# Kernel optimization log

Hardware: AMD Instinct MI355X
Metric: run time of the kernel (lower is better)

## Reference

```python
import jax, jax.numpy as jnp
import numpy as np

N = 100000      # nodes
E = 1600000     # edges (before self loops)
IN_DIM, EMB, HID, OUT, L = 128, 128, 128, 64, 3
LN_EPS = 1e-5


def _lin(k, fi, fo):
    return (jax.random.normal(k, (fi, fo), jnp.float32) / np.sqrt(fi)).astype(jnp.float32)


def setup_inputs() -> dict:
    key = jax.random.key(0)
    ks = jax.random.split(key, 8)
    x = jax.random.normal(ks[0], (N, IN_DIM), jnp.float32)
    edge_index = jax.random.randint(ks[1], (2, E), 0, N, dtype=jnp.int64)
    # in-degree of destination nodes (as data.degree would provide)
    degree = jnp.zeros((N,), jnp.float32).at[edge_index[1]].add(1.0)
    lks = jax.random.split(ks[2], 2 * L)
    W1 = jnp.stack([_lin(lks[2 * i], EMB, HID) for i in range(L)])
    W2 = jnp.stack([_lin(lks[2 * i + 1], HID, EMB) for i in range(L)])
    return dict(
        x=x, edge_index=edge_index, degree=degree,
        Win=_lin(ks[3], IN_DIM, EMB), b_in=jnp.zeros((EMB,), jnp.float32),
        W1=W1, b1=jnp.zeros((L, HID), jnp.float32),
        W2=W2, b2=jnp.zeros((L, EMB), jnp.float32),
        ln_g=jnp.ones((L, EMB), jnp.float32), ln_b=jnp.zeros((L, EMB), jnp.float32),
        out_g=jnp.ones((EMB,), jnp.float32), out_b=jnp.zeros((EMB,), jnp.float32),
        Wout=_lin(ks[4], EMB, OUT), b_out=jnp.zeros((OUT,), jnp.float32),
    )


def _layernorm(h, g, b):
    m = h.mean(-1, keepdims=True)
    v = ((h - m) ** 2).mean(-1, keepdims=True)
    return (h - m) * jax.lax.rsqrt(v + LN_EPS) * g + b


def reference(x, edge_index, degree, Win, b_in, W1, b1, W2, b2,
              ln_g, ln_b, out_g, out_b, Wout, b_out):
    # input_lin: Linear -> Dropout(eval: identity) -> ReLU
    h = jax.nn.relu(x @ Win + b_in)                        # [N, EMB]
    # add self loops, degree + 1
    loop = jnp.arange(N, dtype=edge_index.dtype)
    src = jnp.concatenate([edge_index[0], loop])           # [E+N]
    dst = jnp.concatenate([edge_index[1], loop])
    inv = jax.lax.rsqrt(degree + 1.0)                      # deg^{-1/2}
    coef = (inv[src] * inv[dst])[:, None]                  # symmetric GCN norm
    for i in range(L):
        m = h @ W1[i] + b1[i]                              # [N, HID]
        agg = jax.ops.segment_sum(m[src] * coef, dst, num_segments=N)  # gather-scatter
        out = agg @ W2[i] + b2[i]                          # [N, EMB]
        h = jax.nn.relu(_layernorm(out + h, ln_g[i], ln_b[i]))  # residual + LN + act (dropout=id)
    h = _layernorm(h, out_g, out_b)
    return h @ Wout + b_out
```

## Files before the change

### kernel.cpp

```cpp
#include <hip/hip_runtime.h>
#include <cstdint>
#include <cstddef>

typedef unsigned short u16;
typedef unsigned int u32;
typedef __attribute__((ext_vector_type(2))) unsigned short u16x2;
typedef __attribute__((ext_vector_type(4))) unsigned short u16x4;
typedef __attribute__((ext_vector_type(8))) unsigned short u16x8;
typedef __attribute__((ext_vector_type(8))) __bf16 bf16x8;
typedef __attribute__((ext_vector_type(4))) float f32x4;

#define PREP_F32   0
#define PREP_BF16  1
#define PREP_LN    2
#define EPI_IN    0
#define EPI_SCALE 1
#define EPI_NONE  3

__device__ __forceinline__ float wred(float v) {
#pragma unroll
  for (int m = 32; m >= 1; m >>= 1) v += __shfl_xor(v, m, 64);
  return v;
}
__device__ __forceinline__ u16 f2bf(float f) {
  u32 u = __float_as_uint(f);
  u += 0x7fffu + ((u >> 16) & 1u);
  return (u16)(u >> 16);
}
__device__ __forceinline__ float bflo(u32 u) { return __uint_as_float(u << 16); }
__device__ __forceinline__ float bfhi(u32 u) { return __uint_as_float(u & 0xffff0000u); }
__device__ __forceinline__ u32 pack2(float a, float b) {
  u32 ua = __float_as_uint(a); ua += 0x7fffu + ((ua >> 16) & 1u);
  u32 ub = __float_as_uint(b); ub += 0x7fffu + ((ub >> 16) & 1u);
  return (ua >> 16) | (ub & 0xffff0000u);
}


template <int NOUT, int PREP, int EPI>
__device__ __forceinline__ void gemm_body(
    const void* __restrict__ Xv, const u16* __restrict__ Wp,
    const float* __restrict__ bias, void* __restrict__ Yv,
    const void* __restrict__ resv, const float* __restrict__ g1,
    const float* __restrict__ lb1, int N, int bid) {
  constexpr int NT = NOUT / 16;
  __shared__ union {
    u16  xs[32][136];
    float cs[32][132];
  } sh;
  const int tid = threadIdx.x;
  const int lane = tid & 63, wid = tid >> 6;
  const int row0 = bid * 32;

  if constexpr (PREP == PREP_F32) {
    const float* X = (const float*)Xv;
    for (int i = tid; i < 1024; i += 256) {
      int r = i >> 5, c4 = i & 31;
      float4 v = ((const float4*)(X + (size_t)(row0 + r) * 128))[c4];
      u16x4 o = {f2bf(v.x), f2bf(v.y), f2bf(v.z), f2bf(v.w)};
      *(u16x4*)&sh.xs[r][c4 * 4] = o;
    }
  } else if constexpr (PREP == PREP_BF16) {
    const u16x4* X = (const u16x4*)Xv;
    for (int i = tid; i < 1024; i += 256) {
      int r = i >> 5, c4 = i & 31;
      *(u16x4*)&sh.xs[r][c4 * 4] = X[(size_t)(row0 + r) * 32 + c4];
    }
  } else {
    const u32* X = (const u32*)Xv;
    float2 gg = *(const float2*)&g1[lane * 2];
    float2 bb = *(const float2*)&lb1[lane * 2];
    for (int rr = 0; rr < 8; ++rr) {
      int r = wid * 8 + rr;
      u32 v = X[(size_t)(row0 + r) * 64 + lane];
      float tx = bflo(v), ty = bfhi(v);
      float mean = wred(tx + ty) * (1.f / 128.f);
      float dx = tx - mean, dy = ty - mean;
      float var = wred(dx * dx + dy * dy) * (1.f / 128.f);
      float rstd = rsqrtf(var + 1e-5f);
      u16x2 o = {f2bf(dx * rstd * gg.x + bb.x), f2bf(dy * rstd * gg.y + bb.y)};
      *(u16x2*)&sh.xs[r][lane * 2] = o;
    }
  }
  __syncthreads();

  constexpr int NTW = (NOUT == 128) ? 4 : 2;
  const int m0  = (NOUT == 128) ? ((wid >> 1) << 4) : ((wid & 1) << 4);
  const int ntb = (NOUT == 128) ? ((wid & 1) << 2) : ((wid >> 1) << 1);

  f32x4 acc[NTW];
#pragma unroll
  for (int t = 0; t < NTW; ++t) acc[t] = (f32x4){0.f, 0.f, 0.f, 0.f};

  const int ar  = m0 + (lane & 15);
  const int akb = (lane >> 4) << 2;
  const bf16x8* Bp = (const bf16x8*)Wp;
#pragma unroll
  for (int kc = 0; kc < 4; ++kc) {
    u16x4 lo = *(const u16x4*)&sh.xs[ar][kc * 32 + akb];
    u16x4 hi = *(const u16x4*)&sh.xs[ar][kc * 32 + akb + 16];
    u16x8 av;
#pragma unroll
    for (int j = 0; j < 4; ++j) { av[j] = lo[j]; av[j + 4] = hi[j]; }
    bf16x8 a = __builtin_bit_cast(bf16x8, av);
#pragma unroll
    for (int t = 0; t < NTW; ++t) {
      bf16x8 b = Bp[(kc * NT + ntb + t) * 64 + lane];
      acc[t] = __builtin_amdgcn_mfma_f32_16x16x32_bf16(a, b, acc[t], 0, 0, 0);
    }
  }

  const int cb = lane & 15;
  const int rg = (lane >> 4) << 2;
  if constexpr (EPI == EPI_NONE) {
    float* Y = (float*)Yv;
#pragma unroll
    for (int t = 0; t < NTW; ++t) {
      int col = (ntb + t) * 16 + cb;
      float bv = bias[col];
#pragma unroll
      for (int r = 0; r < 4; ++r) {
        int gr = row0 + m0 + rg + r;
        Y[(size_t)gr * NOUT + col] = acc[t][r] + bv;
      }
    }
  } else if constexpr (EPI == EPI_SCALE) {
    const float* inv = (const float*)resv;
    u16* Y = (u16*)Yv;
#pragma unroll
    for (int t = 0; t < NTW; ++t) {
      int col = (ntb + t) * 16 + cb;
      float bv = bias[col];
#pragma unroll
      for (int r = 0; r < 4; ++r) {
        int gr = row0 + m0 + rg + r;
        Y[(size_t)gr * NOUT + col] = f2bf((acc[t][r] + bv) * inv[gr]);
      }
    }
  } else {
    __syncthreads();
#pragma unroll
    for (int t = 0; t < NTW; ++t) {
      int col = (ntb + t) * 16 + cb;
      float bv = bias[col];
#pragma unroll
      for (int r = 0; r < 4; ++r) sh.cs[m0 + rg + r][col] = acc[t][r] + bv;
    }
    __syncthreads();
    u32* Y = (u32*)Yv;
    for (int rr = 0; rr < 8; ++rr) {
      int r = wid * 8 + rr;
      int gr = row0 + r;
      float2 t2 = *(const float2*)&sh.cs[r][lane * 2];
      Y[(size_t)gr * 64 + lane] = pack2(fmaxf(t2.x, 0.f), fmaxf(t2.y, 0.f));
    }
  }
}


__global__ __launch_bounds__(256) void d1_scan_pack_k(
    const float* __restrict__ deg, int* __restrict__ offs,
    int* __restrict__ bsum, float* __restrict__ inv, int N, int nb,
    const float* __restrict__ Win, const float* __restrict__ W1,
    const float* __restrict__ W2, const float* __restrict__ Wout,
    u16* __restrict__ pWin, u16* __restrict__ pW1,
    u16* __restrict__ pW2, u16* __restrict__ pWout) {
  if ((int)blockIdx.x < nb) {
    __shared__ int sh[256];
    int tid = threadIdx.x;
    int i = blockIdx.x * 256 + tid;
    int c = (i < N) ? (int)(deg[i] + 0.5f) : 0;
    if (i < N) inv[i] = rsqrtf(deg[i] + 1.0f);
    int val = c;
    for (int off = 1; off < 256; off <<= 1) {
      sh[tid] = val; __syncthreads();
      if (tid >= off) val += sh[tid - off];
      __syncthreads();
    }
    if (i < N) offs[i] = val - c;
    if (tid == 255) bsum[blockIdx.x] = val;
    return;
  }
  const int b = blockIdx.x - nb;
  const float* W; u16* P; int ncol; int t;
  if (b < 8)       { W = Win;                        P = pWin;                      ncol = 128; t = b * 256 + threadIdx.x; }
  else if (b < 32) { int l = (b - 8) / 8;  W = W1 + (size_t)l * 16384;  P = pW1 + (size_t)l * 16384; ncol = 128; t = ((b - 8) % 8) * 256 + threadIdx.x; }
  else if (b < 56) { int l = (b - 32) / 8; W = W2 + (size_t)l * 16384;  P = pW2 + (size_t)l * 16384; ncol = 128; t = ((b - 32) % 8) * 256 + threadIdx.x; }
  else             { W = Wout;                       P = pWout;                     ncol = 64;  t = (b - 56) * 256 + threadIdx.x; }
  int NT = ncol >> 4;
  int total = 4 * NT * 64;
  if (t >= total) return;
  int lane = t & 63;
  int tmp = t >> 6;
  int nt = tmp % NT, kc = tmp / NT;
  int n = nt * 16 + (lane & 15);
  int kb = kc * 32 + ((lane >> 4) << 2);
  u16* dst = P + (size_t)t * 8;
#pragma unroll
  for (int j = 0; j < 8; ++j) {
    int k = kb + (j & 3) + ((j >> 2) << 4);
    dst[j] = f2bf(W[(size_t)k * ncol + n]);
  }
}

__global__ __launch_bounds__(256) void d2_gemmin_bsum_k(
    const void* __restrict__ Xv, const u16* __restrict__ Wp,
    const float* __restrict__ bias, void* __restrict__ Yv, int N,
    int* __restrict__ bsum, int nb) {
  if (blockIdx.x == gridDim.x - 1) {
    __shared__ int a[512], b[512];
    int tid = threadIdx.x;
    for (int i = tid; i < 512; i += 256) a[i] = (i < nb) ? bsum[i] : 0;
    __syncthreads();
    int* src = a; int* dst = b;
    for (int off = 1; off < 512; off <<= 1) {
      for (int i = tid; i < 512; i += 256)
        dst[i] = (i >= off) ? src[i] + src[i - off] : src[i];
      __syncthreads();
      int* t = src; src = dst; dst = t;
    }
    for (int i = tid; i < nb; i += 256) bsum[i] = (i > 0) ? src[i - 1] : 0;
    return;
  }
  gemm_body<128, PREP_F32, EPI_IN>(Xv, Wp, bias, Yv, nullptr, nullptr, nullptr,
                                   N, blockIdx.x);
}

__global__ __launch_bounds__(256) void d3_gemmscale_scanadd_k(
    const void* __restrict__ Xv, const u16* __restrict__ Wp,
    const float* __restrict__ bias, void* __restrict__ Yv,
    const float* __restrict__ inv, int N,
    int* __restrict__ offs, const int* __restrict__ bsum,
    int* __restrict__ gcur, int E, int gemmGrid) {
  if ((int)blockIdx.x >= gemmGrid) {
    int i = (blockIdx.x - gemmGrid) * 256 + threadIdx.x;
    if (i < N) {
      int o = offs[i] + bsum[i >> 8];
      offs[i] = o;
      if ((i & 511) == 0) gcur[i >> 9] = o;
    } else if (i == N) {
      offs[N] = E;
    }
    return;
  }
  gemm_body<128, PREP_BF16, EPI_SCALE>(Xv, Wp, bias, Yv, inv, nullptr, nullptr,
                                       N, blockIdx.x);
}

template <int NOUT, int PREP, int EPI>
__global__ __launch_bounds__(256) void gemm_mfma(
    const void* __restrict__ Xv, const u16* __restrict__ Wp,
    const float* __restrict__ bias, void* __restrict__ Yv,
    const void* __restrict__ resv, const float* __restrict__ g1,
    const float* __restrict__ lb1, int N) {
  gemm_body<NOUT, PREP, EPI>(Xv, Wp, bias, Yv, resv, g1, lb1, N, blockIdx.x);
}

__global__ __launch_bounds__(256) void scatter_k(
    const int* __restrict__ src, const int* __restrict__ dst,
    int* __restrict__ gcur, u32* __restrict__ pairs, int E) {
  __shared__ int hist[256];
  __shared__ int base_[256];
  const int tid = threadIdx.x;
  const int e0 = blockIdx.x * 8192;
  const int e1 = min(E, e0 + 8192);
  hist[tid] = 0;
  __syncthreads();
  for (int e = e0 + tid; e < e1; e += 256)
    atomicAdd(&hist[dst[e] >> 9], 1);
  __syncthreads();
  int c = hist[tid];
  if (c > 0) base_[tid] = atomicAdd(&gcur[tid], c);
  hist[tid] = 0;
  __syncthreads();
  for (int e = e0 + tid; e < e1; e += 256) {
    int d = dst[e];
    int b = d >> 9;
    int r = atomicAdd(&hist[b], 1);
    pairs[base_[b] + r] = (u32)src[e] | ((u32)(d & 511) << 17);
  }
}

__global__ __launch_bounds__(256) void fill2_k(
    const u32* __restrict__ pairs, const int* __restrict__ offs,
    int* __restrict__ col, int N) {
  __shared__ int cur[512];
  const int b = blockIdx.x;
  const int n0 = b << 9;
  const int n1 = min(N, n0 + 512);
  const int tid = threadIdx.x;
  for (int i = tid; i < n1 - n0; i += 256) cur[i] = offs[n0 + i];
  __syncthreads();
  const int e0 = offs[n0], e1 = offs[n1];
  for (int e = e0 + tid; e < e1; e += 256) {
    u32 pr = pairs[e];
    int p = atomicAdd(&cur[pr >> 17], 1);
    col[p] = (int)(pr & 0x1FFFFu);
  }
}

__global__ __launch_bounds__(256) void spmm_gemm_k(
    const uint4* __restrict__ msc, const int* __restrict__ offs,
    const int* __restrict__ col, const float* __restrict__ inv,
    const u16* __restrict__ Wp, const float* __restrict__ bias,
    u32* __restrict__ h, const float* __restrict__ g1,
    const float* __restrict__ lb1, int N) {
  __shared__ union {
    u16  xs[32][136];
    float cs[16][132];
  } sh;
  const int tid = threadIdx.x;
  const int lane = tid & 63, wid = tid >> 6;
  const int row0 = blockIdx.x * 32;
  const int rgrp = lane >> 4, c = lane & 15;

#pragma unroll
  for (int p = 0; p < 2; ++p) {
    const int lrow = wid * 8 + p * 4 + rgrp;
    const int d = row0 + lrow;
    const int s0 = offs[d], s1 = offs[d + 1];
    const int last = s1 - 1;
    float2 a0 = {0.f, 0.f}, a1 = {0.f, 0.f}, a2 = {0.f, 0.f}, a3 = {0.f, 0.f};
    for (int k = s0; k < s1; k += 8) {
      int sv[8];
#pragma unroll
      for (int j = 0; j < 8; ++j) sv[j] = col[min(k + j, last)];
      uint4 rv[8];
#pragma unroll
      for (int j = 0; j < 8; ++j) rv[j] = msc[(size_t)sv[j] * 16 + c];
#pragma unroll
      for (int j = 0; j < 8; ++j) {
        float m = (k + j < s1) ? 1.f : 0.f;
        a0.x = fmaf(m, bflo(rv[j].x), a0.x); a0.y = fmaf(m, bfhi(rv[j].x), a0.y);
        a1.x = fmaf(m, bflo(rv[j].y), a1.x); a1.y = fmaf(m, bfhi(rv[j].y), a1.y);
        a2.x = fmaf(m, bflo(rv[j].z), a2.x); a2.y = fmaf(m, bfhi(rv[j].z), a2.y);
        a3.x = fmaf(m, bflo(rv[j].w), a3.x); a3.y = fmaf(m, bfhi(rv[j].w), a3.y);
      }
    }
    uint4 r = msc[(size_t)d * 16 + c];
    float iv = inv[d];
    uint4 o;
    o.x = pack2((a0.x + bflo(r.x)) * iv, (a0.y + bfhi(r.x)) * iv);
    o.y = pack2((a1.x + bflo(r.y)) * iv, (a1.y + bfhi(r.y)) * iv);
    o.z = pack2((a2.x + bflo(r.z)) * iv, (a2.y + bfhi(r.z)) * iv);
    o.w = pack2((a3.x + bflo(r.w)) * iv, (a3.y + bfhi(r.w)) * iv);
    *(uint4*)&sh.xs[lrow][c * 8] = o;
  }
  __syncthreads();

  const int m0  = (wid >> 1) << 4;
  const int ntb = (wid & 1) << 2;
  f32x4 acc[4];
#pragma unroll
  for (int t = 0; t < 4; ++t) acc[t] = (f32x4){0.f, 0.f, 0.f, 0.f};
  const int ar  = m0 + (lane & 15);
  const int akb = (lane >> 4) << 2;
  const bf16x8* Bp = (const bf16x8*)Wp;
#pragma unroll
  for (int kc = 0; kc < 4; ++kc) {
    u16x4 lo = *(const u16x4*)&sh.xs[ar][kc * 32 + akb];
    u16x4 hi = *(const u16x4*)&sh.xs[ar][kc * 32 + akb + 16];
    u16x8 av;
#pragma unroll
    for (int j = 0; j < 4; ++j) { av[j] = lo[j]; av[j + 4] = hi[j]; }
    bf16x8 a = __builtin_bit_cast(bf16x8, av);
#pragma unroll
    for (int t = 0; t < 4; ++t) {
      bf16x8 b = Bp[(kc * 8 + ntb + t) * 64 + lane];
      acc[t] = __builtin_amdgcn_mfma_f32_16x16x32_bf16(a, b, acc[t], 0, 0, 0);
    }
  }

  const int cb = lane & 15;
  const int rg = (lane >> 4) << 2;
  float2 gg = *(const float2*)&g1[lane * 2];
  float2 bb = *(const float2*)&lb1[lane * 2];
#pragma unroll
  for (int hh = 0; hh < 2; ++hh) {
    __syncthreads();
    if ((m0 >> 4) == hh) {
#pragma unroll
      for (int t = 0; t < 4; ++t) {
        int colm = (ntb + t) * 16 + cb;
        float bv = bias[colm];
#pragma unroll
        for (int r = 0; r < 4; ++r) sh.cs[rg + r][colm] = acc[t][r] + bv;
      }
    }
    __syncthreads();
    for (int rr = 0; rr < 4; ++rr) {
      int lr = wid * 4 + rr;
      int gr = row0 + hh * 16 + lr;
      float2 t2 = *(const float2*)&sh.cs[lr][lane * 2];
      u32 hv = h[(size_t)gr * 64 + lane];
      float tx = t2.x + bflo(hv), ty = t2.y + bfhi(hv);
      float mean = wred(tx + ty) * (1.f / 128.f);
      float dx = tx - mean, dy = ty - mean;
      float var = wred(dx * dx + dy * dy) * (1.f / 128.f);
      float rstd = rsqrtf(var + 1e-5f);
      float y0 = fmaxf(dx * rstd * gg.x + bb.x, 0.f);
      float y1 = fmaxf(dy * rstd * gg.y + bb.y, 0.f);
      h[(size_t)gr * 64 + lane] = pack2(y0, y1);
    }
  }
}

extern "C" void kernel_launch(void* const* d_in, const int* in_sizes, int n_in,
                              void* d_out, int out_size, void* d_ws, size_t ws_size,
                              hipStream_t stream) {
  (void)n_in; (void)out_size; (void)ws_size;
  const float* x      = (const float*)d_in[0];
  const int*   eidx   = (const int*)d_in[1];
  const float* degree = (const float*)d_in[2];
  const float* Win    = (const float*)d_in[3];
  const float* b_in   = (const float*)d_in[4];
  const float* W1     = (const float*)d_in[5];
  const float* b1     = (const float*)d_in[6];
  const float* W2     = (const float*)d_in[7];
  const float* b2     = (const float*)d_in[8];
  const float* ln_g   = (const float*)d_in[9];
  const float* ln_b   = (const float*)d_in[10];
  const float* out_g  = (const float*)d_in[11];
  const float* out_b  = (const float*)d_in[12];
  const float* Wout   = (const float*)d_in[13];
  const float* b_out  = (const float*)d_in[14];

  const int N = in_sizes[0] / 128;
  const int E = in_sizes[1] / 2;
  const int* esrc = eidx;
  const int* edst = eidx + E;

  char* p = (char*)d_ws;
  auto alloc = [&](size_t bytes) {
    char* q = p;
    p += (bytes + 255) & ~(size_t)255;
    return q;
  };
  float* inv    = (float*)alloc((size_t)N * 4);
  int*   offs   = (int*)alloc(((size_t)N + 1) * 4);
  int*   gcur   = (int*)alloc(256 * 4);
  int*   bsum   = (int*)alloc(1024 * 4);
  int*   col    = (int*)alloc((size_t)E * 4);
  u32*   pairs  = (u32*)alloc((size_t)E * 4);
  u32*   h      = (u32*)alloc((size_t)N * 128 * 2);
  u32*   msc    = (u32*)alloc((size_t)N * 128 * 2);
  u16*   pWin   = (u16*)alloc(4 * 8 * 64 * 8 * 2);
  u16*   pWout  = (u16*)alloc(4 * 4 * 64 * 8 * 2);
  u16*   pW1    = (u16*)alloc(3 * 4 * 8 * 64 * 8 * 2);
  u16*   pW2    = (u16*)alloc(3 * 4 * 8 * 64 * 8 * 2);

  const int nb = (N + 255) / 256;
  const int NB = (N + 511) / 512;
  const int gemmGrid = (N + 31) / 32;
  const int saGrid = (N + 256) / 256;

  d1_scan_pack_k<<<nb + 60, 256, 0, stream>>>(
      degree, offs, bsum, inv, N, nb,
      Win, W1, W2, Wout, pWin, pW1, pW2, pWout);
  d2_gemmin_bsum_k<<<gemmGrid + 1, 256, 0, stream>>>(
      x, pWin, b_in, h, N, bsum, nb);
  d3_gemmscale_scanadd_k<<<gemmGrid + saGrid, 256, 0, stream>>>(
      h, pW1, b1, msc, inv, N, offs, bsum, gcur, E, gemmGrid);
  scatter_k<<<(E + 8191) / 8192, 256, 0, stream>>>(esrc, edst, gcur, pairs, E);
  fill2_k<<<NB, 256, 0, stream>>>(pairs, offs, col, N);

  spmm_gemm_k<<<gemmGrid, 256, 0, stream>>>(
      (const uint4*)msc, offs, col, inv, pW2, b2, h, ln_g, ln_b, N);
  for (int l = 1; l < 3; ++l) {
    gemm_mfma<128, PREP_BF16, EPI_SCALE><<<gemmGrid, 256, 0, stream>>>(
        h, pW1 + (size_t)l * 16384, b1 + l * 128, msc, inv, nullptr, nullptr, N);
    spmm_gemm_k<<<gemmGrid, 256, 0, stream>>>(
        (const uint4*)msc, offs, col, inv, pW2 + (size_t)l * 16384,
        b2 + l * 128, h, ln_g + l * 128, ln_b + l * 128, N);
  }
  gemm_mfma<64, PREP_LN, EPI_NONE><<<gemmGrid, 256, 0, stream>>>(
      h, pWout, b_out, d_out, nullptr, out_g, out_b, N);
}
```

Baseline: 362.7 us.

## Fuse next-layer W1 GEMM and final LN+output GEMM into SpMM layer kernel

Each SpMM+W2+LayerNorm kernel now keeps the normalized rows in shared memory and immediately runs the next layer's W1 GEMM (with inv scaling) or, for the last layer, the output LayerNorm and Wout projection. The input projection kernel likewise chains directly into the first W1 GEMM. The scan-add work is split into its own small kernel. This removes several kernel launches and the re-read of h from global memory between stages, at the cost of double-buffered message arrays and more shared memory and registers per block.

```diff
diff --git a/kernel.cpp b/kernel.cpp
--- a/kernel.cpp
+++ b/kernel.cpp
@@ -10,13 +10,6 @@
 typedef __attribute__((ext_vector_type(8))) __bf16 bf16x8;
 typedef __attribute__((ext_vector_type(4))) float f32x4;
 
-#define PREP_F32   0
-#define PREP_BF16  1
-#define PREP_LN    2
-#define EPI_IN    0
-#define EPI_SCALE 1
-#define EPI_NONE  3
-
 __device__ __forceinline__ float wred(float v) {
 #pragma unroll
   for (int m = 32; m >= 1; m >>= 1) v += __shfl_xor(v, m, 64);
@@ -35,127 +28,25 @@
   return (ua >> 16) | (ub & 0xffff0000u);
 }
 
-
-template <int NOUT, int PREP, int EPI>
-__device__ __forceinline__ void gemm_body(
-    const void* __restrict__ Xv, const u16* __restrict__ Wp,
-    const float* __restrict__ bias, void* __restrict__ Yv,
-    const void* __restrict__ resv, const float* __restrict__ g1,
-    const float* __restrict__ lb1, int N, int bid) {
-  constexpr int NT = NOUT / 16;
-  __shared__ union {
-    u16  xs[32][136];
-    float cs[32][132];
-  } sh;
-  const int tid = threadIdx.x;
-  const int lane = tid & 63, wid = tid >> 6;
-  const int row0 = bid * 32;
-
-  if constexpr (PREP == PREP_F32) {
-    const float* X = (const float*)Xv;
-    for (int i = tid; i < 1024; i += 256) {
-      int r = i >> 5, c4 = i & 31;
-      float4 v = ((const float4*)(X + (size_t)(row0 + r) * 128))[c4];
-      u16x4 o = {f2bf(v.x), f2bf(v.y), f2bf(v.z), f2bf(v.w)};
-      *(u16x4*)&sh.xs[r][c4 * 4] = o;
-    }
-  } else if constexpr (PREP == PREP_BF16) {
-    const u16x4* X = (const u16x4*)Xv;
-    for (int i = tid; i < 1024; i += 256) {
-      int r = i >> 5, c4 = i & 31;
-      *(u16x4*)&sh.xs[r][c4 * 4] = X[(size_t)(row0 + r) * 32 + c4];
-    }
-  } else {
-    const u32* X = (const u32*)Xv;
-    float2 gg = *(const float2*)&g1[lane * 2];
-    float2 bb = *(const float2*)&lb1[lane * 2];
-    for (int rr = 0; rr < 8; ++rr) {
-      int r = wid * 8 + rr;
-      u32 v = X[(size_t)(row0 + r) * 64 + lane];
-      float tx = bflo(v), ty = bfhi(v);
-      float mean = wred(tx + ty) * (1.f / 128.f);
-      float dx = tx - mean, dy = ty - mean;
-      float var = wred(dx * dx + dy * dy) * (1.f / 128.f);
-      float rstd = rsqrtf(var + 1e-5f);
-      u16x2 o = {f2bf(dx * rstd * gg.x + bb.x), f2bf(dy * rstd * gg.y + bb.y)};
-      *(u16x2*)&sh.xs[r][lane * 2] = o;
-    }
-  }
-  __syncthreads();
-
-  constexpr int NTW = (NOUT == 128) ? 4 : 2;
-  const int m0  = (NOUT == 128) ? ((wid >> 1) << 4) : ((wid & 1) << 4);
-  const int ntb = (NOUT == 128) ? ((wid & 1) << 2) : ((wid >> 1) << 1);
-
-  f32x4 acc[NTW];
-#pragma unroll
-  for (int t = 0; t < NTW; ++t) acc[t] = (f32x4){0.f, 0.f, 0.f, 0.f};
-
-  const int ar  = m0 + (lane & 15);
-  const int akb = (lane >> 4) << 2;
-  const bf16x8* Bp = (const bf16x8*)Wp;
-#pragma unroll
-  for (int kc = 0; kc < 4; ++kc) {
-    u16x4 lo = *(const u16x4*)&sh.xs[ar][kc * 32 + akb];
-    u16x4 hi = *(const u16x4*)&sh.xs[ar][kc * 32 + akb + 16];
-    u16x8 av;
-#pragma unroll
-    for (int j = 0; j < 4; ++j) { av[j] = lo[j]; av[j + 4] = hi[j]; }
-    bf16x8 a = __builtin_bit_cast(bf16x8, av);
-#pragma unroll
-    for (int t = 0; t < NTW; ++t) {
-      bf16x8 b = Bp[(kc * NT + ntb + t) * 64 + lane];
-      acc[t] = __builtin_amdgcn_mfma_f32_16x16x32_bf16(a, b, acc[t], 0, 0, 0);
-    }
-  }
-
-  const int cb = lane & 15;
-  const int rg = (lane >> 4) << 2;
-  if constexpr (EPI == EPI_NONE) {
-    float* Y = (float*)Yv;
-#pragma unroll
-    for (int t = 0; t < NTW; ++t) {
-      int col = (ntb + t) * 16 + cb;
-      float bv = bias[col];
-#pragma unroll
-      for (int r = 0; r < 4; ++r) {
-        int gr = row0 + m0 + rg + r;
-        Y[(size_t)gr * NOUT + col] = acc[t][r] + bv;
-      }
-    }
-  } else if constexpr (EPI == EPI_SCALE) {
-    const float* inv = (const float*)resv;
-    u16* Y = (u16*)Yv;
-#pragma unroll
-    for (int t = 0; t < NTW; ++t) {
-      int col = (ntb + t) * 16 + cb;
-      float bv = bias[col];
-#pragma unroll
-      for (int r = 0; r < 4; ++r) {
-        int gr = row0 + m0 + rg + r;
-        Y[(size_t)gr * NOUT + col] = f2bf((acc[t][r] + bv) * inv[gr]);
-      }
-    }
-  } else {
-    __syncthreads();
-#pragma unroll
-    for (int t = 0; t < NTW; ++t) {
-      int col = (ntb + t) * 16 + cb;
-      float bv = bias[col];
-#pragma unroll
-      for (int r = 0; r < 4; ++r) sh.cs[m0 + rg + r][col] = acc[t][r] + bv;
-    }
-    __syncthreads();
-    u32* Y = (u32*)Yv;
-    for (int rr = 0; rr < 8; ++rr) {
-      int r = wid * 8 + rr;
-      int gr = row0 + r;
-      float2 t2 = *(const float2*)&sh.cs[r][lane * 2];
-      Y[(size_t)gr * 64 + lane] = pack2(fmaxf(t2.x, 0.f), fmaxf(t2.y, 0.f));
-    }
-  }
-}
-
+#define MFMA128_FROM_XS(ACC, BP)                                               \
+  {                                                                            \
+    const int ar_ = m0 + (lane & 15);                                          \
+    const int akb_ = (lane >> 4) << 2;                                         \
+    _Pragma("unroll")                                                          \
+    for (int kc = 0; kc < 4; ++kc) {                                           \
+      u16x4 lo = *(const u16x4*)&xs[ar_][kc * 32 + akb_];                      \
+      u16x4 hi = *(const u16x4*)&xs[ar_][kc * 32 + akb_ + 16];                 \
+      u16x8 av;                                                                \
+      _Pragma("unroll")                                                        \
+      for (int j = 0; j < 4; ++j) { av[j] = lo[j]; av[j + 4] = hi[j]; }        \
+      bf16x8 a = __builtin_bit_cast(bf16x8, av);                               \
+      _Pragma("unroll")                                                        \
+      for (int t = 0; t < 4; ++t) {                                            \
+        bf16x8 b = (BP)[(kc * 8 + ntb + t) * 64 + lane];                       \
+        (ACC)[t] = __builtin_amdgcn_mfma_f32_16x16x32_bf16(a, b, (ACC)[t], 0, 0, 0); \
+      }                                                                        \
+    }                                                                          \
+  }
 
 __global__ __launch_bounds__(256) void d1_scan_pack_k(
     const float* __restrict__ deg, int* __restrict__ offs,
@@ -202,16 +93,18 @@
   }
 }
 
-__global__ __launch_bounds__(256) void d2_gemmin_bsum_k(
-    const void* __restrict__ Xv, const u16* __restrict__ Wp,
-    const float* __restrict__ bias, void* __restrict__ Yv, int N,
+__global__ __launch_bounds__(256) void in_scale_k(
+    const float* __restrict__ x, const u16* __restrict__ pWin,
+    const float* __restrict__ b_in, const u16* __restrict__ pW1,
+    const float* __restrict__ b1, const float* __restrict__ inv,
+    u32* __restrict__ h, u16* __restrict__ msc, int N,
     int* __restrict__ bsum, int nb) {
   if (blockIdx.x == gridDim.x - 1) {
-    __shared__ int a[512], b[512];
+    __shared__ int a_[512], b_[512];
     int tid = threadIdx.x;
-    for (int i = tid; i < 512; i += 256) a[i] = (i < nb) ? bsum[i] : 0;
+    for (int i = tid; i < 512; i += 256) a_[i] = (i < nb) ? bsum[i] : 0;
     __syncthreads();
-    int* src = a; int* dst = b;
+    int* src = a_; int* dst = b_;
     for (int off = 1; off < 512; off <<= 1) {
       for (int i = tid; i < 512; i += 256)
         dst[i] = (i >= off) ? src[i] + src[i - off] : src[i];
@@ -221,38 +114,83 @@
     for (int i = tid; i < nb; i += 256) bsum[i] = (i > 0) ? src[i - 1] : 0;
     return;
   }
-  gemm_body<128, PREP_F32, EPI_IN>(Xv, Wp, bias, Yv, nullptr, nullptr, nullptr,
-                                   N, blockIdx.x);
-}
-
-__global__ __launch_bounds__(256) void d3_gemmscale_scanadd_k(
-    const void* __restrict__ Xv, const u16* __restrict__ Wp,
-    const float* __restrict__ bias, void* __restrict__ Yv,
-    const float* __restrict__ inv, int N,
-    int* __restrict__ offs, const int* __restrict__ bsum,
-    int* __restrict__ gcur, int E, int gemmGrid) {
-  if ((int)blockIdx.x >= gemmGrid) {
-    int i = (blockIdx.x - gemmGrid) * 256 + threadIdx.x;
-    if (i < N) {
-      int o = offs[i] + bsum[i >> 8];
-      offs[i] = o;
-      if ((i & 511) == 0) gcur[i >> 9] = o;
-    } else if (i == N) {
-      offs[N] = E;
-    }
-    return;
-  }
-  gemm_body<128, PREP_BF16, EPI_SCALE>(Xv, Wp, bias, Yv, inv, nullptr, nullptr,
-                                       N, blockIdx.x);
-}
-
-template <int NOUT, int PREP, int EPI>
-__global__ __launch_bounds__(256) void gemm_mfma(
-    const void* __restrict__ Xv, const u16* __restrict__ Wp,
-    const float* __restrict__ bias, void* __restrict__ Yv,
-    const void* __restrict__ resv, const float* __restrict__ g1,
-    const float* __restrict__ lb1, int N) {
-  gemm_body<NOUT, PREP, EPI>(Xv, Wp, bias, Yv, resv, g1, lb1, N, blockIdx.x);
+  __shared__ u16 xs[32][136];
+  __shared__ float cs[16][132];
+  const int tid = threadIdx.x;
+  const int lane = tid & 63, wid = tid >> 6;
+  const int row0 = blockIdx.x * 32;
+
+  for (int i = tid; i < 1024; i += 256) {
+    int r = i >> 5, c4 = i & 31;
+    float4 v = ((const float4*)(x + (size_t)(row0 + r) * 128))[c4];
+    u16x4 o = {f2bf(v.x), f2bf(v.y), f2bf(v.z), f2bf(v.w)};
+    *(u16x4*)&xs[r][c4 * 4] = o;
+  }
+  __syncthreads();
+
+  const int m0  = (wid >> 1) << 4;
+  const int ntb = (wid & 1) << 2;
+  f32x4 acc[4];
+#pragma unroll
+  for (int t = 0; t < 4; ++t) acc[t] = (f32x4){0.f, 0.f, 0.f, 0.f};
+  MFMA128_FROM_XS(acc, (const bf16x8*)pWin);
+
+  const int cb = lane & 15;
+  const int rg = (lane >> 4) << 2;
+#pragma unroll
+  for (int hh = 0; hh < 2; ++hh) {
+    __syncthreads();
+    if ((m0 >> 4) == hh) {
+#pragma unroll
+      for (int t = 0; t < 4; ++t) {
+        int colm = (ntb + t) * 16 + cb;
+        float bv = b_in[colm];
+#pragma unroll
+        for (int r = 0; r < 4; ++r) cs[rg + r][colm] = acc[t][r] + bv;
+      }
+    }
+    __syncthreads();
+    for (int rr = 0; rr < 4; ++rr) {
+      int lr = wid * 4 + rr;
+      int r = hh * 16 + lr;
+      int gr = row0 + r;
+      float2 t2 = *(const float2*)&cs[lr][lane * 2];
+      u32 pk = pack2(fmaxf(t2.x, 0.f), fmaxf(t2.y, 0.f));
+      h[(size_t)gr * 64 + lane] = pk;
+      *(u32*)&xs[r][lane * 2] = pk;
+    }
+  }
+  __syncthreads();
+
+  f32x4 acc2[4];
+#pragma unroll
+  for (int t = 0; t < 4; ++t) acc2[t] = (f32x4){0.f, 0.f, 0.f, 0.f};
+  MFMA128_FROM_XS(acc2, (const bf16x8*)pW1);
+  float iv4[4];
+#pragma unroll
+  for (int r = 0; r < 4; ++r) iv4[r] = inv[row0 + m0 + rg + r];
+#pragma unroll
+  for (int t = 0; t < 4; ++t) {
+    int colm = (ntb + t) * 16 + cb;
+    float bv = b1[colm];
+#pragma unroll
+    for (int r = 0; r < 4; ++r) {
+      int gr = row0 + m0 + rg + r;
+      msc[(size_t)gr * 128 + colm] = f2bf((acc2[t][r] + bv) * iv4[r]);
+    }
+  }
+}
+
+__global__ void scan_add_k(int* __restrict__ offs, const int* __restrict__ bsum,
+                           int* __restrict__ gcur, int N, int E) {
+  int i = blockIdx.x * 256 + threadIdx.x;
+  if (i < N) {
+    int o = offs[i] + bsum[i >> 8];
+    offs[i] = o;
+    if ((i & 511) == 0) gcur[i >> 9] = o;
+  } else if (i == N) {
+    offs[N] = E;
+  }
 }
 
 __global__ __launch_bounds__(256) void scatter_k(
@@ -298,16 +236,18 @@
   }
 }
 
-__global__ __launch_bounds__(256) void spmm_gemm_k(
-    const uint4* __restrict__ msc, const int* __restrict__ offs,
+template <int FINAL>
+__global__ __launch_bounds__(256) void layer_fused_k(
+    const uint4* __restrict__ mscin, const int* __restrict__ offs,
     const int* __restrict__ col, const float* __restrict__ inv,
-    const u16* __restrict__ Wp, const float* __restrict__ bias,
+    const u16* __restrict__ pW2, const float* __restrict__ b2,
     u32* __restrict__ h, const float* __restrict__ g1,
-    const float* __restrict__ lb1, int N) {
-  __shared__ union {
-    u16  xs[32][136];
-    float cs[16][132];
-  } sh;
+    const float* __restrict__ lb1,
+    const u16* __restrict__ pWn, const float* __restrict__ bn,
+    void* __restrict__ outv, const float* __restrict__ og,
+    const float* __restrict__ ob, int N) {
+  __shared__ u16 xs[32][136];
+  __shared__ float cs[16][132];
   const int tid = threadIdx.x;
   const int lane = tid & 63, wid = tid >> 6;
   const int row0 = blockIdx.x * 32;
@@ -326,7 +266,7 @@
       for (int j = 0; j < 8; ++j) sv[j] = col[min(k + j, last)];
       uint4 rv[8];
 #pragma unroll
-      for (int j = 0; j < 8; ++j) rv[j] = msc[(size_t)sv[j] * 16 + c];
+      for (int j = 0; j < 8; ++j) rv[j] = mscin[(size_t)sv[j] * 16 + c];
 #pragma unroll
       for (int j = 0; j < 8; ++j) {
         float m = (k + j < s1) ? 1.f : 0.f;
@@ -336,14 +276,14 @@
         a3.x = fmaf(m, bflo(rv[j].w), a3.x); a3.y = fmaf(m, bfhi(rv[j].w), a3.y);
       }
     }
-    uint4 r = msc[(size_t)d * 16 + c];
+    uint4 r = mscin[(size_t)d * 16 + c];
     float iv = inv[d];
     uint4 o;
     o.x = pack2((a0.x + bflo(r.x)) * iv, (a0.y + bfhi(r.x)) * iv);
     o.y = pack2((a1.x + bflo(r.y)) * iv, (a1.y + bfhi(r.y)) * iv);
     o.z = pack2((a2.x + bflo(r.z)) * iv, (a2.y + bfhi(r.z)) * iv);
     o.w = pack2((a3.x + bflo(r.w)) * iv, (a3.y + bfhi(r.w)) * iv);
-    *(uint4*)&sh.xs[lrow][c * 8] = o;
+    *(uint4*)&xs[lrow][c * 8] = o;
   }
   __syncthreads();
 
@@ -352,28 +292,17 @@
   f32x4 acc[4];
 #pragma unroll
   for (int t = 0; t < 4; ++t) acc[t] = (f32x4){0.f, 0.f, 0.f, 0.f};
-  const int ar  = m0 + (lane & 15);
-  const int akb = (lane >> 4) << 2;
-  const bf16x8* Bp = (const bf16x8*)Wp;
-#pragma unroll
-  for (int kc = 0; kc < 4; ++kc) {
-    u16x4 lo = *(const u16x4*)&sh.xs[ar][kc * 32 + akb];
-    u16x4 hi = *(const u16x4*)&sh.xs[ar][kc * 32 + akb + 16];
-    u16x8 av;
-#pragma unroll
-    for (int j = 0; j < 4; ++j) { av[j] = lo[j]; av[j + 4] = hi[j]; }
-    bf16x8 a = __builtin_bit_cast(bf16x8, av);
-#pragma unroll
-    for (int t = 0; t < 4; ++t) {
-      bf16x8 b = Bp[(kc * 8 + ntb + t) * 64 + lane];
-      acc[t] = __builtin_amdgcn_mfma_f32_16x16x32_bf16(a, b, acc[t], 0, 0, 0);
-    }
-  }
+  MFMA128_FROM_XS(acc, (const bf16x8*)pW2);
 
   const int cb = lane & 15;
   const int rg = (lane >> 4) << 2;
   float2 gg = *(const float2*)&g1[lane * 2];
   float2 bb = *(const float2*)&lb1[lane * 2];
+  float2 ogg, obb;
+  if constexpr (FINAL) {
+    ogg = *(const float2*)&og[lane * 2];
+    obb = *(const float2*)&ob[lane * 2];
+  }
 #pragma unroll
   for (int hh = 0; hh < 2; ++hh) {
     __syncthreads();
@@ -381,16 +310,17 @@
 #pragma unroll
       for (int t = 0; t < 4; ++t) {
         int colm = (ntb + t) * 16 + cb;
-        float bv = bias[colm];
-#pragma unroll
-        for (int r = 0; r < 4; ++r) sh.cs[rg + r][colm] = acc[t][r] + bv;
+        float bv = b2[colm];
+#pragma unroll
+        for (int r = 0; r < 4; ++r) cs[rg + r][colm] = acc[t][r] + bv;
       }
     }
     __syncthreads();
     for (int rr = 0; rr < 4; ++rr) {
       int lr = wid * 4 + rr;
-      int gr = row0 + hh * 16 + lr;
-      float2 t2 = *(const float2*)&sh.cs[lr][lane * 2];
+      int r = hh * 16 + lr;
+      int gr = row0 + r;
+      float2 t2 = *(const float2*)&cs[lr][lane * 2];
       u32 hv = h[(size_t)gr * 64 + lane];
       float tx = t2.x + bflo(hv), ty = t2.y + bfhi(hv);
       float mean = wred(tx + ty) * (1.f / 128.f);
@@ -399,7 +329,74 @@
       float rstd = rsqrtf(var + 1e-5f);
       float y0 = fmaxf(dx * rstd * gg.x + bb.x, 0.f);
       float y1 = fmaxf(dy * rstd * gg.y + bb.y, 0.f);
-      h[(size_t)gr * 64 + lane] = pack2(y0, y1);
+      if constexpr (!FINAL) {
+        u32 pk = pack2(y0, y1);
+        h[(size_t)gr * 64 + lane] = pk;
+        *(u32*)&xs[r][lane * 2] = pk;
+      } else {
+        float m2 = wred(y0 + y1) * (1.f / 128.f);
+        float dx2 = y0 - m2, dy2 = y1 - m2;
+        float v2 = wred(dx2 * dx2 + dy2 * dy2) * (1.f / 128.f);
+        float rs2 = rsqrtf(v2 + 1e-5f);
+        *(u32*)&xs[r][lane * 2] =
+            pack2(dx2 * rs2 * ogg.x + obb.x, dy2 * rs2 * ogg.y + obb.y);
+      }
+    }
+  }
+  __syncthreads();
+
+  if constexpr (!FINAL) {
+    f32x4 acc2[4];
+#pragma unroll
+    for (int t = 0; t < 4; ++t) acc2[t] = (f32x4){0.f, 0.f, 0.f, 0.f};
+    MFMA128_FROM_XS(acc2, (const bf16x8*)pWn);
+    u16* Y = (u16*)outv;
+    float iv4[4];
+#pragma unroll
+    for (int r = 0; r < 4; ++r) iv4[r] = inv[row0 + m0 + rg + r];
+#pragma unroll
+    for (int t = 0; t < 4; ++t) {
+      int colm = (ntb + t) * 16 + cb;
+      float bv = bn[colm];
+#pragma unroll
+      for (int r = 0; r < 4; ++r) {
+        int gr = row0 + m0 + rg + r;
+        Y[(size_t)gr * 128 + colm] = f2bf((acc2[t][r] + bv) * iv4[r]);
+      }
+    }
+  } else {
+    const int m0b = (wid & 1) << 4;
+    const int ntbb = (wid >> 1) << 1;
+    const int arb = m0b + (lane & 15);
+    const int akb = (lane >> 4) << 2;
+    f32x4 acc2[2];
+#pragma unroll
+    for (int t = 0; t < 2; ++t) acc2[t] = (f32x4){0.f, 0.f, 0.f, 0.f};
+    const bf16x8* Bp = (const bf16x8*)pWn;
+#pragma unroll
+    for (int kc = 0; kc < 4; ++kc) {
+      u16x4 lo = *(const u16x4*)&xs[arb][kc * 32 + akb];
+      u16x4 hi = *(const u16x4*)&xs[arb][kc * 32 + akb + 16];
+      u16x8 av;
+#pragma unroll
+      for (int j = 0; j < 4; ++j) { av[j] = lo[j]; av[j + 4] = hi[j]; }
+      bf16x8 a = __builtin_bit_cast(bf16x8, av);
+#pragma unroll
+      for (int t = 0; t < 2; ++t) {
+        bf16x8 b = Bp[(kc * 4 + ntbb + t) * 64 + lane];
+        acc2[t] = __builtin_amdgcn_mfma_f32_16x16x32_bf16(a, b, acc2[t], 0, 0, 0);
+      }
+    }
+    float* Y = (float*)outv;
+#pragma unroll
+    for (int t = 0; t < 2; ++t) {
+      int colo = (ntbb + t) * 16 + cb;
+      float bv = bn[colo];
+#pragma unroll
+      for (int r = 0; r < 4; ++r) {
+        int gr = row0 + m0b + rg + r;
+        Y[(size_t)gr * 64 + colo] = acc2[t][r] + bv;
+      }
     }
   }
 }
@@ -442,7 +439,8 @@
   int*   col    = (int*)alloc((size_t)E * 4);
   u32*   pairs  = (u32*)alloc((size_t)E * 4);
   u32*   h      = (u32*)alloc((size_t)N * 128 * 2);
-  u32*   msc    = (u32*)alloc((size_t)N * 128 * 2);
+  u32*   mscA   = (u32*)alloc((size_t)N * 128 * 2);
+  u32*   mscB   = (u32*)alloc((size_t)N * 128 * 2);
   u16*   pWin   = (u16*)alloc(4 * 8 * 64 * 8 * 2);
   u16*   pWout  = (u16*)alloc(4 * 4 * 64 * 8 * 2);
   u16*   pW1    = (u16*)alloc(3 * 4 * 8 * 64 * 8 * 2);
@@ -456,22 +454,19 @@
   d1_scan_pack_k<<<nb + 60, 256, 0, stream>>>(
       degree, offs, bsum, inv, N, nb,
       Win, W1, W2, Wout, pWin, pW1, pW2, pWout);
-  d2_gemmin_bsum_k<<<gemmGrid + 1, 256, 0, stream>>>(
-      x, pWin, b_in, h, N, bsum, nb);
-  d3_gemmscale_scanadd_k<<<gemmGrid + saGrid, 256, 0, stream>>>(
-      h, pW1, b1, msc, inv, N, offs, bsum, gcur, E, gemmGrid);
+  in_scale_k<<<gemmGrid + 1, 256, 0, stream>>>(
+      x, pWin, b_in, pW1, b1, inv, h, (u16*)mscA, N, bsum, nb);
+  scan_add_k<<<saGrid, 256, 0, stream>>>(offs, bsum, gcur, N, E);
   scatter_k<<<(E + 8191) / 8192, 256, 0, stream>>>(esrc, edst, gcur, pairs, E);
   fill2_k<<<NB, 256, 0, stream>>>(pairs, offs, col, N);
 
-  spmm_gemm_k<<<gemmGrid, 256, 0, stream>>>(
-      (const uint4*)msc, offs, col, inv, pW2, b2, h, ln_g, ln_b, N);
-  for (int l = 1; l < 3; ++l) {
-    gemm_mfma<128, PREP_BF16, EPI_SCALE><<<gemmGrid, 256, 0, stream>>>(
-        h, pW1 + (size_t)l * 16384, b1 + l * 128, msc, inv, nullptr, nullptr, N);
-    spmm_gemm_k<<<gemmGrid, 256, 0, stream>>>(
-        (const uint4*)msc, offs, col, inv, pW2 + (size_t)l * 16384,
-        b2 + l * 128, h, ln_g + l * 128, ln_b + l * 128, N);
-  }
-  gemm_mfma<64, PREP_LN, EPI_NONE><<<gemmGrid, 256, 0, stream>>>(
-      h, pWout, b_out, d_out, nullptr, out_g, out_b, N);
-}
+  layer_fused_k<0><<<gemmGrid, 256, 0, stream>>>(
+      (const uint4*)mscA, offs, col, inv, pW2, b2, h, ln_g, ln_b,
+      pW1 + 16384, b1 + 128, mscB, nullptr, nullptr, N);
+  layer_fused_k<0><<<gemmGrid, 256, 0, stream>>>(
+      (const uint4*)mscB, offs, col, inv, pW2 + 16384, b2 + 128, h,
+      ln_g + 128, ln_b + 128, pW1 + 32768, b1 + 256, mscA, nullptr, nullptr, N);
+  layer_fused_k<1><<<gemmGrid, 256, 0, stream>>>(
+      (const uint4*)mscA, offs, col, inv, pW2 + 32768, b2 + 256, h,
+      ln_g + 256, ln_b + 256, pWout, b_out, d_out, out_g, out_b, N);
+}
```

Result: faster. 333.9 us (-8.0%).
